# Performance work log

Measured on AMD Instinct MI355X. Metric: run time of the kernel, lower is better.

The kernel has to match this reference:

```python
import jax, jax.numpy as jnp
import numpy as np

# db4 decomposition filters (pywt convention)
DB4_LO = np.array([-0.010597401784997278, 0.032883011666982945, 0.030841381835986965,
                   -0.18703481171888114, -0.02798376941698385, 0.6308807679295904,
                   0.7148465705525415, 0.23037781330885523], dtype=np.float32)
DB4_HI = np.array([-0.23037781330885523, 0.7148465705525415, -0.6308807679295904,
                   -0.02798376941698385, 0.18703481171888114, 0.030841381835986965,
                   -0.032883011666982945, -0.010597401784997278], dtype=np.float32)
PAD = 3


def setup_inputs() -> dict:
    key = jax.random.key(0)
    x = jax.random.normal(key, (4, 3, 32, 256, 256), dtype=jnp.float32)
    filt = jnp.stack([jnp.asarray(DB4_LO), jnp.asarray(DB4_HI)])  # [2, 8]
    return {"x": x, "filt": filt}


def _dwt1d(x, filt, axis):
    """Analysis filter bank along one axis: reflect-pad, true convolution
    with (dec_lo, dec_hi), stride 2. Returns (low, high) with that axis halved."""
    x = jnp.moveaxis(x, axis, -1)
    shp = x.shape
    L = shp[-1]
    x2 = x.reshape(-1, 1, L)
    x2 = jnp.pad(x2, ((0, 0), (0, 0), (PAD, PAD)), mode="reflect")
    # flip filters so lax correlation == mathematical convolution with dec filters
    k = jnp.flip(filt, axis=-1)[:, None, :]  # [2, 1, 8]
    y = jax.lax.conv_general_dilated(
        x2, k, window_strides=(2,), padding="VALID",
        dimension_numbers=("NCH", "OIH", "NCH"))  # [N, 2, L//2]
    y = y.reshape(shp[:-1] + (2, L // 2))
    lo = jnp.moveaxis(y[..., 0, :], -1, axis)
    hi = jnp.moveaxis(y[..., 1, :], -1, axis)
    return lo, hi


def reference(x, filt):
    # x: [B, C, T, H, W] -> [B, 8C, T/2, H/2, W/2]
    lo_t, hi_t = _dwt1d(x, filt, 2)
    subbands = []
    for a in (lo_t, hi_t):
        lo_h, hi_h = _dwt1d(a, filt, 3)
        for b in (lo_h, hi_h):
            lo_w, hi_w = _dwt1d(b, filt, 4)
            subbands.append(lo_w)
            subbands.append(hi_w)
    # order: LLL, LLH, LHL, LHH, HLL, HLH, HHL, HHH (t,h,w)
    return jnp.concatenate(subbands, axis=1)
```

## Files before the change

### kernel.cpp

```cpp
#include <hip/hip_runtime.h>
#include <hip/hip_bf16.h>


#define CC 3
#define TT 32
#define HH 256
#define WW 256
#define TOH 16
#define HOH 128
#define WOH 128

#define TH 4
#define TW 32
#define NROWS 14
#define RSLOT 72
#define RSLOT2 36
#define NSLOTS 8
#define DEPTH 6
#define NW 8
#define NTHREADS 512
#define VSTR 512
#define NRR (4*NROWS)
#define NIT (NRR/2)

constexpr float GLO[8] = {
     0.23037781330885523f,  0.7148465705525415f,   0.6308807679295904f,
    -0.02798376941698385f, -0.18703481171888114f,  0.030841381835986965f,
     0.032883011666982945f, -0.010597401784997278f };
constexpr float GHI[8] = {
    -0.010597401784997278f, -0.032883011666982945f, 0.030841381835986965f,
     0.18703481171888114f,  -0.02798376941698385f,  -0.6308807679295904f,
     0.7148465705525415f,   -0.23037781330885523f };

__device__ __forceinline__ int refl(int p, int n) {
    p = p < 0 ? -p : p;
    p = p >= n ? 2 * n - 2 - p : p;
    return p;
}

__global__ __launch_bounds__(NTHREADS)
void dwt3d_db4_kernel(const float* __restrict__ x, float* __restrict__ out) {
    __shared__ float Ring[NW * NSLOTS * RSLOT];
    __shared__ __hip_bfloat16 Vbuf[TT * VSTR];

    const int tid  = threadIdx.x;
    const int wid  = tid >> 6;
    const int lane = tid & 63;
    const int wo   = lane & 31;
    const int p    = lane >> 5;

    const int lin = blockIdx.x;
    const int nid = (lin & 7) * 192 + (lin >> 3);
    const int wo0 = (nid & 3) * TW;
    const int ho0 = ((nid >> 2) & 31) * TH;
    const int bz  = nid >> 7;
    const int b = bz / CC, c = bz - b * CC;

    const float* xs = x + (size_t)bz * (TT * HH * WW);

    const int gcol0 = refl(2 * wo0 - 3 + lane, WW);
    const int gcol1 = refl(2 * wo0 + 3 + lane, WW);

    float wH0[4], wH1[4];
#pragma unroll
    for (int d = 0; d < 4; ++d) {
        wH0[d] = p ? GLO[2 * d + 1] : GLO[2 * d];
        wH1[d] = p ? GHI[2 * d + 1] : GHI[2 * d];
    }

    const int t0 = wid * 4;
    const int ringbase = wid * (NSLOTS * RSLOT);
    const float2* Ring2 = (const float2*)Ring;
    const int r2base = wid * (NSLOTS * RSLOT2) + p * RSLOT2 + wo;
    const int vcolbase = p * 128 + wo;

#define ISSUE(rr_) do {                                                       \
        const int t_ = (rr_) / NROWS, r_ = (rr_) % NROWS;                     \
        const int gr_ = refl(2 * ho0 - 3 + r_, HH);                           \
        const float* rowp_ = xs + (size_t)(t0 + t_) * (HH * WW) + gr_ * WW;   \
        float* lp_ = &Ring[ringbase + ((rr_) & (NSLOTS - 1)) * RSLOT];        \
        __builtin_amdgcn_global_load_lds(                                     \
            (const __attribute__((address_space(1))) void*)(rowp_ + gcol0),   \
            (__attribute__((address_space(3))) void*)lp_, 4, 0, 0);           \
        __builtin_amdgcn_global_load_lds(                                     \
            (const __attribute__((address_space(1))) void*)(rowp_ + gcol1),   \
            (__attribute__((address_space(3))) void*)(lp_ + 6), 4, 0, 0);     \
    } while (0)

    float vacc0[2][4], vacc1[2][4];
#pragma unroll
    for (int sh = 0; sh < 2; ++sh)
#pragma unroll
        for (int ho = 0; ho < 4; ++ho) { vacc0[sh][ho] = 0.f; vacc1[sh][ho] = 0.f; }

#pragma unroll
    for (int rr = 0; rr < DEPTH; ++rr) ISSUE(rr);

#pragma unroll
    for (int k = 0; k < NIT; ++k) {
        if (k <= 25)      asm volatile("s_waitcnt vmcnt(8)" ::: "memory");
        else if (k == 26) asm volatile("s_waitcnt vmcnt(4)" ::: "memory");
        else              asm volatile("s_waitcnt vmcnt(0)" ::: "memory");

        const int soff = ((2 * k) & (NSLOTS - 1)) * RSLOT2;
        const float2 d0 = Ring2[r2base + soff + 0];
        const float2 d1 = Ring2[r2base + soff + 1];
        const float2 d2 = Ring2[r2base + soff + 2];
        const float2 d3 = Ring2[r2base + soff + 3];

        float m_lo, m_hi;
        {
            float a0 = d0.x, a1 = d0.y, a2 = d1.x, a3 = d1.y;
            float a4 = d2.x, a5 = d2.y, a6 = d3.x, a7 = d3.y;
            m_lo = a0 * GLO[0]; m_hi = a0 * GHI[0];
            m_lo = fmaf(a1, GLO[1], m_lo); m_hi = fmaf(a1, GHI[1], m_hi);
            m_lo = fmaf(a2, GLO[2], m_lo); m_hi = fmaf(a2, GHI[2], m_hi);
            m_lo = fmaf(a3, GLO[3], m_lo); m_hi = fmaf(a3, GHI[3], m_hi);
            m_lo = fmaf(a4, GLO[4], m_lo); m_hi = fmaf(a4, GHI[4], m_hi);
            m_lo = fmaf(a5, GLO[5], m_lo); m_hi = fmaf(a5, GHI[5], m_hi);
            m_lo = fmaf(a6, GLO[6], m_lo); m_hi = fmaf(a6, GHI[6], m_hi);
            m_lo = fmaf(a7, GLO[7], m_lo); m_hi = fmaf(a7, GHI[7], m_hi);
        }

        if (2 * k + 6 < NRR) { ISSUE(2 * k + 6); ISSUE(2 * k + 7); }

        const int kk = k % 7;
#pragma unroll
        for (int ho = 0; ho < 4; ++ho) {
            const int d = kk - ho;
            if (d >= 0 && d < 4) {
                vacc0[0][ho] = fmaf(m_lo, wH0[d], vacc0[0][ho]);
                vacc0[1][ho] = fmaf(m_lo, wH1[d], vacc0[1][ho]);
                vacc1[0][ho] = fmaf(m_hi, wH0[d], vacc1[0][ho]);
                vacc1[1][ho] = fmaf(m_hi, wH1[d], vacc1[1][ho]);
            }
        }

        if (kk == 6) {
            const int t = t0 + k / 7;
#pragma unroll
            for (int sh = 0; sh < 2; ++sh)
#pragma unroll
                for (int ho = 0; ho < 4; ++ho) {
                    const float send = p ? vacc0[sh][ho] : vacc1[sh][ho];
                    const float keep = p ? vacc1[sh][ho] : vacc0[sh][ho];
                    const float recv = __shfl_xor(send, 32, 64);
                    Vbuf[t * VSTR + sh * 256 + vcolbase + ho * 32] =
                        __float2bfloat16(keep + recv);
                    vacc0[sh][ho] = 0.f; vacc1[sh][ho] = 0.f;
                }
        }
    }

    __syncthreads();

    float v[TT];
#pragma unroll
    for (int t = 0; t < TT; ++t) v[t] = __bfloat162float(Vbuf[t * VSTR + tid]);

    const int subhw = tid >> 7;
    const int hoq   = (tid >> 5) & 3;
    const int wo2   = tid & 31;

    const size_t hw = (size_t)(ho0 + hoq) * WOH + (wo0 + wo2);
    const size_t ch_lo = (size_t)(subhw * CC + c);
    const size_t ch_hi = (size_t)((4 + subhw) * CC + c);
    const size_t o_lo = (((size_t)b * 24 + ch_lo) * TOH) * (HOH * WOH) + hw;
    const size_t o_hi = (((size_t)b * 24 + ch_hi) * TOH) * (HOH * WOH) + hw;

#pragma unroll
    for (int to = 0; to < TOH; ++to) {
        float lo = 0.f, hi = 0.f;
#pragma unroll
        for (int j = 0; j < 8; ++j) {
            int q = 2 * to + j - 3;
            q = q < 0 ? -q : q;
            q = q >= TT ? 2 * TT - 2 - q : q;
            lo = fmaf(v[q], GLO[j], lo);
            hi = fmaf(v[q], GHI[j], hi);
        }
        out[o_lo + (size_t)to * (HOH * WOH)] = lo;
        out[o_hi + (size_t)to * (HOH * WOH)] = hi;
    }
}

extern "C" void kernel_launch(void* const* d_in, const int* in_sizes, int n_in,
                              void* d_out, int out_size, void* d_ws, size_t ws_size,
                              hipStream_t stream) {
    (void)in_sizes; (void)n_in; (void)d_ws; (void)ws_size; (void)out_size;
    const float* x = (const float*)d_in[0];
    float* out = (float*)d_out;
    dim3 grid(1536, 1, 1);
    dim3 block(NTHREADS);
    hipLaunchKernelGGL(dwt3d_db4_kernel, grid, block, 0, stream, x, out);
}
```

Measured before the change: 43.87 us.

## Replace LDS ring with direct per-lane float2 register loads, double-buffered

Drops the async global_load_lds ring buffer and its manual vmcnt waits. Each lane now loads its 10-float window straight into registers as five float2 reads, double-buffered across the P/Q register sets so the next row loads while the current one computes. Reflect padding at the left and right tile edges is handled by per-lane element remapping instead of reflected column indices. This removes the LDS round trip and per-row LDS reads, but lanes now load overlapping windows (redundant global/L1 traffic), prefetch depth drops to a single row, and the boundary remap adds branches.

```diff
diff --git a/kernel.cpp b/kernel.cpp
--- a/kernel.cpp
+++ b/kernel.cpp
@@ -9,19 +9,10 @@
 #define TOH 16
 #define HOH 128
 #define WOH 128
-
 #define TH 4
 #define TW 32
-#define NROWS 14
-#define RSLOT 72
-#define RSLOT2 36
-#define NSLOTS 8
-#define DEPTH 6
-#define NW 8
 #define NTHREADS 512
 #define VSTR 512
-#define NRR (4*NROWS)
-#define NIT (NRR/2)
 
 constexpr float GLO[8] = {
      0.23037781330885523f,  0.7148465705525415f,   0.6308807679295904f,
@@ -40,7 +31,6 @@
 
 __global__ __launch_bounds__(NTHREADS)
 void dwt3d_db4_kernel(const float* __restrict__ x, float* __restrict__ out) {
-    __shared__ float Ring[NW * NSLOTS * RSLOT];
     __shared__ __hip_bfloat16 Vbuf[TT * VSTR];
 
     const int tid  = threadIdx.x;
@@ -57,9 +47,11 @@
     const int b = bz / CC, c = bz - b * CC;
 
     const float* xs = x + (size_t)bz * (TT * HH * WW);
+    const int t0 = wid * 4;
 
-    const int gcol0 = refl(2 * wo0 - 3 + lane, WW);
-    const int gcol1 = refl(2 * wo0 + 3 + lane, WW);
+    int gb = 2 * (wo0 + wo) - 4;
+    gb = gb < 0 ? 0 : (gb > 246 ? 246 : gb);
+    const int goff = gb >> 1;
 
     float wH0[4], wH1[4];
 #pragma unroll
@@ -67,25 +59,7 @@
         wH0[d] = p ? GLO[2 * d + 1] : GLO[2 * d];
         wH1[d] = p ? GHI[2 * d + 1] : GHI[2 * d];
     }
-
-    const int t0 = wid * 4;
-    const int ringbase = wid * (NSLOTS * RSLOT);
-    const float2* Ring2 = (const float2*)Ring;
-    const int r2base = wid * (NSLOTS * RSLOT2) + p * RSLOT2 + wo;
     const int vcolbase = p * 128 + wo;
-
-#define ISSUE(rr_) do {                                                       \
-        const int t_ = (rr_) / NROWS, r_ = (rr_) % NROWS;                     \
-        const int gr_ = refl(2 * ho0 - 3 + r_, HH);                           \
-        const float* rowp_ = xs + (size_t)(t0 + t_) * (HH * WW) + gr_ * WW;   \
-        float* lp_ = &Ring[ringbase + ((rr_) & (NSLOTS - 1)) * RSLOT];        \
-        __builtin_amdgcn_global_load_lds(                                     \
-            (const __attribute__((address_space(1))) void*)(rowp_ + gcol0),   \
-            (__attribute__((address_space(3))) void*)lp_, 4, 0, 0);           \
-        __builtin_amdgcn_global_load_lds(                                     \
-            (const __attribute__((address_space(1))) void*)(rowp_ + gcol1),   \
-            (__attribute__((address_space(3))) void*)(lp_ + 6), 4, 0, 0);     \
-    } while (0)
 
     float vacc0[2][4], vacc1[2][4];
 #pragma unroll
@@ -93,64 +67,82 @@
 #pragma unroll
         for (int ho = 0; ho < 4; ++ho) { vacc0[sh][ho] = 0.f; vacc1[sh][ho] = 0.f; }
 
-#pragma unroll
-    for (int rr = 0; rr < DEPTH; ++rr) ISSUE(rr);
+    float2 P0, P1, P2, P3, P4, Q0, Q1, Q2, Q3, Q4;
 
-#pragma unroll
-    for (int k = 0; k < NIT; ++k) {
-        if (k <= 25)      asm volatile("s_waitcnt vmcnt(8)" ::: "memory");
-        else if (k == 26) asm volatile("s_waitcnt vmcnt(4)" ::: "memory");
-        else              asm volatile("s_waitcnt vmcnt(0)" ::: "memory");
+#define ROWF2(k_) ((const float2*)(xs                                         \
+        + (size_t)(t0 + (k_) / 7) * (HH * WW)                                 \
+        + (size_t)refl(2 * ho0 - 3 + 2 * ((k_) % 7) + p, HH) * WW) + goff)
 
-        const int soff = ((2 * k) & (NSLOTS - 1)) * RSLOT2;
-        const float2 d0 = Ring2[r2base + soff + 0];
-        const float2 d1 = Ring2[r2base + soff + 1];
-        const float2 d2 = Ring2[r2base + soff + 2];
-        const float2 d3 = Ring2[r2base + soff + 3];
+#define LOADD(D_, k_) do { const float2* rp_ = ROWF2(k_);                     \
+        (D_##0) = rp_[0]; (D_##1) = rp_[1]; (D_##2) = rp_[2];                 \
+        (D_##3) = rp_[3]; (D_##4) = rp_[4]; } while (0)
 
-        float m_lo, m_hi;
-        {
-            float a0 = d0.x, a1 = d0.y, a2 = d1.x, a3 = d1.y;
-            float a4 = d2.x, a5 = d2.y, a6 = d3.x, a7 = d3.y;
-            m_lo = a0 * GLO[0]; m_hi = a0 * GHI[0];
-            m_lo = fmaf(a1, GLO[1], m_lo); m_hi = fmaf(a1, GHI[1], m_hi);
-            m_lo = fmaf(a2, GLO[2], m_lo); m_hi = fmaf(a2, GHI[2], m_hi);
-            m_lo = fmaf(a3, GLO[3], m_lo); m_hi = fmaf(a3, GHI[3], m_hi);
-            m_lo = fmaf(a4, GLO[4], m_lo); m_hi = fmaf(a4, GHI[4], m_hi);
-            m_lo = fmaf(a5, GLO[5], m_lo); m_hi = fmaf(a5, GHI[5], m_hi);
-            m_lo = fmaf(a6, GLO[6], m_lo); m_hi = fmaf(a6, GHI[6], m_hi);
-            m_lo = fmaf(a7, GLO[7], m_lo); m_hi = fmaf(a7, GHI[7], m_hi);
-        }
+#define COMPUTE(D_, k_) do {                                                  \
+    float a0 = (D_##0).y, a1 = (D_##1).x, a2 = (D_##1).y, a3 = (D_##2).x,     \
+          a4 = (D_##2).y, a5 = (D_##3).x, a6 = (D_##3).y, a7 = (D_##4).x;     \
+    if (wo0 == 0) {                                                           \
+        if (wo == 0) { a0 = (D_##1).y; a1 = (D_##1).x; a2 = (D_##0).y;        \
+                       a3 = (D_##0).x; a4 = (D_##0).y; a5 = (D_##1).x;        \
+                       a6 = (D_##1).y; a7 = (D_##2).x; }                      \
+        else if (wo == 1) { a0 = (D_##0).y; a1 = (D_##0).x; a2 = (D_##0).y;   \
+                            a3 = (D_##1).x; a4 = (D_##1).y; a5 = (D_##2).x;   \
+                            a6 = (D_##2).y; a7 = (D_##3).x; }                 \
+    } else if (wo0 == 96) {                                                   \
+        if (wo == 30) { a0 = (D_##1).y; a1 = (D_##2).x; a2 = (D_##2).y;       \
+                        a3 = (D_##3).x; a4 = (D_##3).y; a5 = (D_##4).x;       \
+                        a6 = (D_##4).y; a7 = (D_##4).x; }                     \
+        else if (wo == 31) { a0 = (D_##2).y; a1 = (D_##3).x; a2 = (D_##3).y;  \
+                             a3 = (D_##4).x; a4 = (D_##4).y; a5 = (D_##4).x;  \
+                             a6 = (D_##3).y; a7 = (D_##3).x; }                \
+    }                                                                         \
+    float m_lo, m_hi;                                                         \
+    m_lo = a0 * GLO[0]; m_hi = a0 * GHI[0];                                   \
+    m_lo = fmaf(a1, GLO[1], m_lo); m_hi = fmaf(a1, GHI[1], m_hi);             \
+    m_lo = fmaf(a2, GLO[2], m_lo); m_hi = fmaf(a2, GHI[2], m_hi);             \
+    m_lo = fmaf(a3, GLO[3], m_lo); m_hi = fmaf(a3, GHI[3], m_hi);             \
+    m_lo = fmaf(a4, GLO[4], m_lo); m_hi = fmaf(a4, GHI[4], m_hi);             \
+    m_lo = fmaf(a5, GLO[5], m_lo); m_hi = fmaf(a5, GHI[5], m_hi);             \
+    m_lo = fmaf(a6, GLO[6], m_lo); m_hi = fmaf(a6, GHI[6], m_hi);             \
+    m_lo = fmaf(a7, GLO[7], m_lo); m_hi = fmaf(a7, GHI[7], m_hi);             \
+    const int kk = (k_) % 7;                                                  \
+    _Pragma("unroll")                                                         \
+    for (int ho = 0; ho < 4; ++ho) {                                          \
+        const int d = kk - ho;                                                \
+        if (d >= 0 && d < 4) {                                                \
+            vacc0[0][ho] = fmaf(m_lo, wH0[d], vacc0[0][ho]);                  \
+            vacc0[1][ho] = fmaf(m_lo, wH1[d], vacc0[1][ho]);                  \
+            vacc1[0][ho] = fmaf(m_hi, wH0[d], vacc1[0][ho]);                  \
+            vacc1[1][ho] = fmaf(m_hi, wH1[d], vacc1[1][ho]);                  \
+        }                                                                     \
+    }                                                                         \
+    if (kk == 6) {                                                            \
+        const int t = t0 + (k_) / 7;                                          \
+        _Pragma("unroll")                                                     \
+        for (int sh = 0; sh < 2; ++sh)                                        \
+            _Pragma("unroll")                                                 \
+            for (int ho = 0; ho < 4; ++ho) {                                  \
+                const float send = p ? vacc0[sh][ho] : vacc1[sh][ho];         \
+                const float keep = p ? vacc1[sh][ho] : vacc0[sh][ho];         \
+                const float recv = __shfl_xor(send, 32, 64);                  \
+                Vbuf[t * VSTR + sh * 256 + vcolbase + ho * 32] =              \
+                    __float2bfloat16(keep + recv);                            \
+                vacc0[sh][ho] = 0.f; vacc1[sh][ho] = 0.f;                     \
+            }                                                                 \
+    }                                                                         \
+} while (0)
 
-        if (2 * k + 6 < NRR) { ISSUE(2 * k + 6); ISSUE(2 * k + 7); }
+#define STEP(CUR_, NXT_, k_) do {                                             \
+        LOADD(NXT_, (k_) + 1); COMPUTE(CUR_, k_); } while (0)
 
-        const int kk = k % 7;
-#pragma unroll
-        for (int ho = 0; ho < 4; ++ho) {
-            const int d = kk - ho;
-            if (d >= 0 && d < 4) {
-                vacc0[0][ho] = fmaf(m_lo, wH0[d], vacc0[0][ho]);
-                vacc0[1][ho] = fmaf(m_lo, wH1[d], vacc0[1][ho]);
-                vacc1[0][ho] = fmaf(m_hi, wH0[d], vacc1[0][ho]);
-                vacc1[1][ho] = fmaf(m_hi, wH1[d], vacc1[1][ho]);
-            }
-        }
-
-        if (kk == 6) {
-            const int t = t0 + k / 7;
-#pragma unroll
-            for (int sh = 0; sh < 2; ++sh)
-#pragma unroll
-                for (int ho = 0; ho < 4; ++ho) {
-                    const float send = p ? vacc0[sh][ho] : vacc1[sh][ho];
-                    const float keep = p ? vacc1[sh][ho] : vacc0[sh][ho];
-                    const float recv = __shfl_xor(send, 32, 64);
-                    Vbuf[t * VSTR + sh * 256 + vcolbase + ho * 32] =
-                        __float2bfloat16(keep + recv);
-                    vacc0[sh][ho] = 0.f; vacc1[sh][ho] = 0.f;
-                }
-        }
-    }
+    LOADD(P, 0);
+    STEP(P, Q, 0);  STEP(Q, P, 1);  STEP(P, Q, 2);  STEP(Q, P, 3);
+    STEP(P, Q, 4);  STEP(Q, P, 5);  STEP(P, Q, 6);  STEP(Q, P, 7);
+    STEP(P, Q, 8);  STEP(Q, P, 9);  STEP(P, Q, 10); STEP(Q, P, 11);
+    STEP(P, Q, 12); STEP(Q, P, 13); STEP(P, Q, 14); STEP(Q, P, 15);
+    STEP(P, Q, 16); STEP(Q, P, 17); STEP(P, Q, 18); STEP(Q, P, 19);
+    STEP(P, Q, 20); STEP(Q, P, 21); STEP(P, Q, 22); STEP(Q, P, 23);
+    STEP(P, Q, 24); STEP(Q, P, 25); STEP(P, Q, 26);
+    COMPUTE(Q, 27);
 
     __syncthreads();
 
```

Result: slower. 63.49 us (+44.7%).
